# Kernel optimization log

Hardware: AMD Instinct MI355X
Metric: run time of the kernel (lower is better)

The kernel has to match this reference:

```python
import jax, jax.numpy as jnp
import numpy as np

NUM_NODES = 100000
EMB_DIM = 64
NUM_EDGES = 1280000
NUM_LAYERS = 3


def setup_inputs() -> dict:
    key = jax.random.key(0)
    k1, k2 = jax.random.split(key)
    edge_index = jax.random.randint(k1, (2, NUM_EDGES), 0, NUM_NODES, dtype=jnp.int32)
    emb = jax.random.normal(k2, (NUM_NODES, EMB_DIM), dtype=jnp.float32) * 0.01
    return {"edge_index": edge_index, "emb": emb}


def _lgconv_norm(edge_index):
    # PyG gcn_norm without self-loops: deg over destination nodes,
    # norm_e = deg[src]^-0.5 * deg[dst]^-0.5
    src, dst = edge_index[0], edge_index[1]
    deg = jax.ops.segment_sum(jnp.ones((edge_index.shape[1],), jnp.float32), dst,
                              num_segments=NUM_NODES)
    dinv = jnp.where(deg > 0, jax.lax.rsqrt(jnp.maximum(deg, 1.0)), 0.0)
    return src, dst, dinv[src] * dinv[dst]


def reference(edge_index, emb):
    src, dst, w = _lgconv_norm(edge_index)
    x = emb
    out = x
    for _ in range(NUM_LAYERS):
        # message: gather source embeddings, scale, scatter-add to destination
        x = jax.ops.segment_sum(x[src] * w[:, None], dst, num_segments=NUM_NODES)
        out = out + x
    return out / (NUM_LAYERS + 1)
```

## Files before the change

### kernel.cpp

```cpp
#include <hip/hip_runtime.h>

#define N_NODES 100000
#define EMB 64
#define N_EDGES 1280000
#define SCAN_TILE 1024

typedef unsigned long long u64;
typedef _Float16 f16;
typedef __attribute__((ext_vector_type(2))) _Float16 f16x2;

__global__ void deg_kernel(const int* __restrict__ dst, int* __restrict__ deg,
                           int* __restrict__ rank) {
    int t = blockIdx.x * blockDim.x + threadIdx.x;
    int e = t * 4;
    if (e + 3 < N_EDGES) {
        int4 d4 = *(const int4*)(dst + e);
        int4 r4;
        r4.x = atomicAdd(&deg[d4.x], 1);
        r4.y = atomicAdd(&deg[d4.y], 1);
        r4.z = atomicAdd(&deg[d4.z], 1);
        r4.w = atomicAdd(&deg[d4.w], 1);
        *(int4*)(rank + e) = r4;
    }
}

__global__ void norm_kernel(const int* __restrict__ deg, float* __restrict__ dinv,
                            float* __restrict__ rdinv) {
    int i = blockIdx.x * blockDim.x + threadIdx.x;
    if (i < N_NODES) {
        int d = deg[i];
        float fd = (float)d;
        dinv[i]  = (d > 0) ? rsqrtf(fd) : 0.0f;
        rdinv[i] = (d > 0) ? sqrtf(fd) : 0.0f;
    }
}

__global__ void y0_kernel(const float* __restrict__ emb, const float* __restrict__ dinv,
                          f16* __restrict__ y0) {
    int i = blockIdx.x * blockDim.x + threadIdx.x;
    const int n4 = N_NODES * EMB / 4;
    if (i < n4) {
        float dv = dinv[i >> 4];
        float4 v = ((const float4*)emb)[i];
        f16 h[4] = {(f16)(v.x * dv), (f16)(v.y * dv), (f16)(v.z * dv), (f16)(v.w * dv)};
        ((u64*)y0)[i] = *(const u64*)h;
    }
}

__global__ void scan1_kernel(const int* __restrict__ deg, int* __restrict__ local_scan,
                             int* __restrict__ block_sums) {
    __shared__ int lds[256];
    int base = blockIdx.x * SCAN_TILE;
    int vals[4];
    int tsum = 0;
#pragma unroll
    for (int k = 0; k < 4; ++k) {
        int i = base + threadIdx.x * 4 + k;
        vals[k] = (i < N_NODES) ? deg[i] : 0;
        tsum += vals[k];
    }
    lds[threadIdx.x] = tsum;
    __syncthreads();
    for (int off = 1; off < 256; off <<= 1) {
        int v = (threadIdx.x >= (unsigned)off) ? lds[threadIdx.x - off] : 0;
        __syncthreads();
        lds[threadIdx.x] += v;
        __syncthreads();
    }
    int texcl = lds[threadIdx.x] - tsum;
    if (threadIdx.x == 255) block_sums[blockIdx.x] = lds[255];
    int run = texcl;
#pragma unroll
    for (int k = 0; k < 4; ++k) {
        int i = base + threadIdx.x * 4 + k;
        if (i < N_NODES) local_scan[i] = run;
        run += vals[k];
    }
}

__global__ void scan2_kernel(int* __restrict__ block_sums, int nb) {
    __shared__ int lds[128];
    int v = (threadIdx.x < (unsigned)nb) ? block_sums[threadIdx.x] : 0;
    lds[threadIdx.x] = v;
    __syncthreads();
    for (int off = 1; off < 128; off <<= 1) {
        int t = (threadIdx.x >= (unsigned)off) ? lds[threadIdx.x - off] : 0;
        __syncthreads();
        lds[threadIdx.x] += t;
        __syncthreads();
    }
    if (threadIdx.x < (unsigned)nb) block_sums[threadIdx.x] = lds[threadIdx.x] - v;
}

__global__ void scan3_kernel(int* __restrict__ row_start, const int* __restrict__ block_sums) {
    int i = blockIdx.x * blockDim.x + threadIdx.x;
    if (i < N_NODES) {
        row_start[i] = row_start[i] + block_sums[i / SCAN_TILE];
    }
    if (i == 0) row_start[N_NODES] = N_EDGES;
}

__global__ void fill_kernel(const int* __restrict__ src, const int* __restrict__ dst,
                            const int* __restrict__ rank, const int* __restrict__ row_start,
                            int* __restrict__ col) {
    int t = blockIdx.x * blockDim.x + threadIdx.x;
    int e = t * 4;
    if (e + 3 < N_EDGES) {
        int4 d4 = *(const int4*)(dst + e);
        int4 r4 = *(const int4*)(rank + e);
        int4 s4 = *(const int4*)(src + e);
        col[row_start[d4.x] + r4.x] = s4.x;
        col[row_start[d4.y] + r4.y] = s4.y;
        col[row_start[d4.z] + r4.z] = s4.z;
        col[row_start[d4.w] + r4.w] = s4.w;
    }
}

template <bool FINAL>
__global__ void gather_kernel(const int* __restrict__ row_start, const int* __restrict__ col,
                              const float* __restrict__ dinv, const float* __restrict__ rdinv,
                              const f16* __restrict__ yin, f16* __restrict__ yout,
                              const float* __restrict__ emb,
                              const f16* __restrict__ y1, const f16* __restrict__ y2,
                              float* __restrict__ out) {
    unsigned int gid = blockIdx.x * blockDim.x + threadIdx.x;
    unsigned int row = gid >> 6;
    int lane = (int)(gid & 63u);
    int s = lane >> 5;
    int j = lane & 31;
    if (row >= N_NODES) return;
    int beg = row_start[row];
    int end = row_start[row + 1];
    const f16* yj = yin + 2 * j;
    float accx = 0.0f, accy = 0.0f;
    for (int cb = beg; cb < end; cb += 64) {
        int idx = cb + lane;
        int ci = 0;
        if (idx < end) ci = col[idx];
        int n = end - cb;
        if (n > 64) n = 64;
        int kk = 0;
        for (; kk + 8 <= n; kk += 8) {
            int c0 = __shfl(ci, kk + s);
            int c1 = __shfl(ci, kk + s + 2);
            int c2 = __shfl(ci, kk + s + 4);
            int c3 = __shfl(ci, kk + s + 6);
            unsigned u0 = *(const unsigned*)(yj + (unsigned)c0 * EMB);
            unsigned u1 = *(const unsigned*)(yj + (unsigned)c1 * EMB);
            unsigned u2 = *(const unsigned*)(yj + (unsigned)c2 * EMB);
            unsigned u3 = *(const unsigned*)(yj + (unsigned)c3 * EMB);
            f16x2 h0 = __builtin_bit_cast(f16x2, u0);
            f16x2 h1 = __builtin_bit_cast(f16x2, u1);
            f16x2 h2 = __builtin_bit_cast(f16x2, u2);
            f16x2 h3 = __builtin_bit_cast(f16x2, u3);
            accx += (float)h0.x + (float)h1.x + (float)h2.x + (float)h3.x;
            accy += (float)h0.y + (float)h1.y + (float)h2.y + (float)h3.y;
        }
        if (kk + 4 <= n) {
            int c0 = __shfl(ci, kk + s);
            int c1 = __shfl(ci, kk + s + 2);
            unsigned u0 = *(const unsigned*)(yj + (unsigned)c0 * EMB);
            unsigned u1 = *(const unsigned*)(yj + (unsigned)c1 * EMB);
            f16x2 h0 = __builtin_bit_cast(f16x2, u0);
            f16x2 h1 = __builtin_bit_cast(f16x2, u1);
            accx += (float)h0.x + (float)h1.x;
            accy += (float)h0.y + (float)h1.y;
            kk += 4;
        }
        for (; kk < n; ++kk) {
            int c = __shfl(ci, kk);
            if (s == (kk & 1)) {
                unsigned u = *(const unsigned*)(yj + (unsigned)c * EMB);
                f16x2 h = __builtin_bit_cast(f16x2, u);
                accx += (float)h.x;
                accy += (float)h.y;
            }
        }
    }
    accx += __shfl_xor(accx, 32);
    accy += __shfl_xor(accy, 32);
    if (s == 0) {
        float dv = dinv[row];
        unsigned int o = row * EMB + 2 * (unsigned)j;
        if (!FINAL) {
            float sc = dv * dv;
            f16x2 h;
            h.x = (f16)(accx * sc);
            h.y = (f16)(accy * sc);
            *(unsigned*)(yout + o) = __builtin_bit_cast(unsigned, h);
        } else {
            float rv = rdinv[row];
            float2 e2 = *(const float2*)(emb + o);
            f16x2 a = __builtin_bit_cast(f16x2, *(const unsigned*)(y1 + o));
            f16x2 b = __builtin_bit_cast(f16x2, *(const unsigned*)(y2 + o));
            float rx = 0.25f * (e2.x + rv * ((float)a.x + (float)b.x) + dv * accx);
            float ry = 0.25f * (e2.y + rv * ((float)a.y + (float)b.y) + dv * accy);
            __builtin_nontemporal_store(rx, out + o);
            __builtin_nontemporal_store(ry, out + o + 1);
        }
    }
}

extern "C" void kernel_launch(void* const* d_in, const int* in_sizes, int n_in,
                              void* d_out, int out_size, void* d_ws, size_t ws_size,
                              hipStream_t stream) {
    const int*   edge = (const int*)d_in[0];
    const int*   src  = edge;
    const int*   dst  = edge + N_EDGES;
    const float* emb  = (const float*)d_in[1];
    float*       out  = (float*)d_out;

    char* ws = (char*)d_ws;
    size_t off = 0;
    int* deg       = (int*)(ws + off); off += 400000;
    int* row_start = (int*)(ws + off); off += 400016;
    int* bsums     = (int*)(ws + off); off += 512;
    float* dinv    = (float*)(ws + off); off += 400000;
    float* rdinv   = (float*)(ws + off); off += 400000;
    int* col       = (int*)(ws + off); off += (size_t)N_EDGES * 4;
    f16* y0        = (f16*)(ws + off); off += (size_t)N_NODES * EMB * 2;
    f16* y1        = (f16*)(ws + off); off += (size_t)N_NODES * EMB * 2;
    f16* y2        = (f16*)(ws + off); off += (size_t)N_NODES * EMB * 2;

    int* rank      = (int*)y1;

    const int NB = (N_NODES + SCAN_TILE - 1) / SCAN_TILE;

    hipMemsetAsync(deg, 0, (size_t)N_NODES * sizeof(int), stream);
    deg_kernel<<<(N_EDGES / 4 + 255) / 256, 256, 0, stream>>>(dst, deg, rank);
    norm_kernel<<<(N_NODES + 255) / 256, 256, 0, stream>>>(deg, dinv, rdinv);
    y0_kernel<<<(N_NODES * EMB / 4 + 255) / 256, 256, 0, stream>>>(emb, dinv, y0);
    scan1_kernel<<<NB, 256, 0, stream>>>(deg, row_start, bsums);
    scan2_kernel<<<1, 128, 0, stream>>>(bsums, NB);
    scan3_kernel<<<(N_NODES + 255) / 256, 256, 0, stream>>>(row_start, bsums);
    fill_kernel<<<(N_EDGES / 4 + 255) / 256, 256, 0, stream>>>(src, dst, rank,
                                                               row_start, col);

    const unsigned int gthreads = (unsigned int)N_NODES * EMB;
    const int gblocks = (int)((gthreads + 255) / 256);
    gather_kernel<false><<<gblocks, 256, 0, stream>>>(row_start, col, dinv, rdinv,
                                                      y0, y1, emb, y1, y2, out);
    gather_kernel<false><<<gblocks, 256, 0, stream>>>(row_start, col, dinv, rdinv,
                                                      y1, y2, emb, y1, y2, out);
    gather_kernel<true><<<gblocks, 256, 0, stream>>>(row_start, col, dinv, rdinv,
                                                     y2, (f16*)0, emb, y1, y2, out);
}
```

Before: 308.4 us.

## Build CSR via two-level bucket sort with LDS-local degree counting

Replaces global-atomic degree counting and a random scatter fill with a bucketed counting sort. Edges are histogrammed into 512-node buckets, scanned, scattered into bucket order, then ranked per bucket with shared-memory atomics that also produce the degree. The CSR fill then reads bucket-ordered edges, so writes to col land in a narrow range. It adds four kernel launches, a single-block scan over roughly 61K entries, and an extra pass over the edge arrays in exchange for avoiding contended global atomics and scattered writes.

Result: slower. 366.2 us (+18.8%).

```diff
diff --git a/kernel.cpp b/kernel.cpp
--- a/kernel.cpp
+++ b/kernel.cpp
@@ -3,24 +3,115 @@
 #define N_NODES 100000
 #define EMB 64
 #define N_EDGES 1280000
+#define N_E4 (N_EDGES / 4)
 #define SCAN_TILE 1024
+
+#define NBUCK 196
+#define BUCK_SHIFT 9
+#define BUCK_NODES 512
+#define EPB 4096
+#define NBA 313
 
 typedef unsigned long long u64;
 typedef _Float16 f16;
 typedef __attribute__((ext_vector_type(2))) _Float16 f16x2;
 
-__global__ void deg_kernel(const int* __restrict__ dst, int* __restrict__ deg,
-                           int* __restrict__ rank) {
-    int t = blockIdx.x * blockDim.x + threadIdx.x;
-    int e = t * 4;
-    if (e + 3 < N_EDGES) {
-        int4 d4 = *(const int4*)(dst + e);
-        int4 r4;
-        r4.x = atomicAdd(&deg[d4.x], 1);
-        r4.y = atomicAdd(&deg[d4.y], 1);
-        r4.z = atomicAdd(&deg[d4.z], 1);
-        r4.w = atomicAdd(&deg[d4.w], 1);
-        *(int4*)(rank + e) = r4;
+__global__ void bucket_hist_kernel(const int* __restrict__ dst, int* __restrict__ hist) {
+    __shared__ int lh[NBUCK];
+    for (int i = threadIdx.x; i < NBUCK; i += 256) lh[i] = 0;
+    __syncthreads();
+#pragma unroll
+    for (int k = 0; k < 4; ++k) {
+        int q = blockIdx.x * 1024 + k * 256 + threadIdx.x;
+        if (q < N_E4) {
+            int4 d4 = ((const int4*)dst)[q];
+            atomicAdd(&lh[d4.x >> BUCK_SHIFT], 1);
+            atomicAdd(&lh[d4.y >> BUCK_SHIFT], 1);
+            atomicAdd(&lh[d4.z >> BUCK_SHIFT], 1);
+            atomicAdd(&lh[d4.w >> BUCK_SHIFT], 1);
+        }
+    }
+    __syncthreads();
+    for (int i = threadIdx.x; i < NBUCK; i += 256)
+        hist[i * NBA + blockIdx.x] = lh[i];
+}
+
+__global__ void bucket_scan_kernel(int* __restrict__ hist) {
+    const int TOT = NBUCK * NBA;
+    __shared__ int lds[1024];
+    int per = (TOT + 1023) / 1024;
+    int beg = threadIdx.x * per;
+    int end = beg + per; if (end > TOT) end = TOT;
+    int s = 0;
+    for (int i = beg; i < end && i < TOT; ++i) s += hist[i];
+    lds[threadIdx.x] = s;
+    __syncthreads();
+    for (int off = 1; off < 1024; off <<= 1) {
+        int v = (threadIdx.x >= (unsigned)off) ? lds[threadIdx.x - off] : 0;
+        __syncthreads();
+        lds[threadIdx.x] += v;
+        __syncthreads();
+    }
+    int run = lds[threadIdx.x] - s;
+    for (int i = beg; i < end && i < TOT; ++i) {
+        int v = hist[i];
+        hist[i] = run;
+        run += v;
+    }
+}
+
+__global__ void bucket_scatter_kernel(const int* __restrict__ src, const int* __restrict__ dst,
+                                      const int* __restrict__ hist,
+                                      int* __restrict__ bsrc, int* __restrict__ bdst) {
+    __shared__ int cur[NBUCK];
+    for (int i = threadIdx.x; i < NBUCK; i += 256)
+        cur[i] = hist[i * NBA + blockIdx.x];
+    __syncthreads();
+#pragma unroll
+    for (int k = 0; k < 4; ++k) {
+        int q = blockIdx.x * 1024 + k * 256 + threadIdx.x;
+        if (q < N_E4) {
+            int4 d4 = ((const int4*)dst)[q];
+            int4 s4 = ((const int4*)src)[q];
+            int p;
+            p = atomicAdd(&cur[d4.x >> BUCK_SHIFT], 1); bsrc[p] = s4.x; bdst[p] = d4.x;
+            p = atomicAdd(&cur[d4.y >> BUCK_SHIFT], 1); bsrc[p] = s4.y; bdst[p] = d4.y;
+            p = atomicAdd(&cur[d4.z >> BUCK_SHIFT], 1); bsrc[p] = s4.z; bdst[p] = d4.z;
+            p = atomicAdd(&cur[d4.w >> BUCK_SHIFT], 1); bsrc[p] = s4.w; bdst[p] = d4.w;
+        }
+    }
+}
+
+__global__ void bucket_rank_kernel(const int* __restrict__ hist, const int* __restrict__ bdst,
+                                   int* __restrict__ brank, int* __restrict__ deg) {
+    __shared__ int lh[BUCK_NODES];
+    int k = blockIdx.x;
+    int beg = hist[k * NBA];
+    int end = (k + 1 < NBUCK) ? hist[(k + 1) * NBA] : N_EDGES;
+    for (int i = threadIdx.x; i < BUCK_NODES; i += 256) lh[i] = 0;
+    __syncthreads();
+    for (int i = beg + threadIdx.x; i < end; i += 256) {
+        int d = bdst[i];
+        brank[i] = atomicAdd(&lh[d & (BUCK_NODES - 1)], 1);
+    }
+    __syncthreads();
+    int nbase = k * BUCK_NODES;
+    for (int i = threadIdx.x; i < BUCK_NODES; i += 256)
+        if (nbase + i < N_NODES) deg[nbase + i] = lh[i];
+}
+
+__global__ void csr_fill_kernel(const int* __restrict__ row_start, const int* __restrict__ bdst,
+                                const int* __restrict__ brank, const int* __restrict__ bsrc,
+                                int* __restrict__ col) {
+    int q = blockIdx.x * blockDim.x + threadIdx.x;
+    if (q < N_E4) {
+        int4 d4 = ((const int4*)bdst)[q];
+        int4 r4 = ((const int4*)brank)[q];
+        int4 s4 = ((const int4*)bsrc)[q];
+        col[row_start[d4.x] + r4.x] = s4.x;
+        col[row_start[d4.y] + r4.y] = s4.y;
+        col[row_start[d4.z] + r4.z] = s4.z;
+        col[row_start[d4.w] + r4.w] = s4.w;
     }
 }
 
@@ -98,22 +189,6 @@
         row_start[i] = row_start[i] + block_sums[i / SCAN_TILE];
     }
     if (i == 0) row_start[N_NODES] = N_EDGES;
-}
-
-__global__ void fill_kernel(const int* __restrict__ src, const int* __restrict__ dst,
-                            const int* __restrict__ rank, const int* __restrict__ row_start,
-                            int* __restrict__ col) {
-    int t = blockIdx.x * blockDim.x + threadIdx.x;
-    int e = t * 4;
-    if (e + 3 < N_EDGES) {
-        int4 d4 = *(const int4*)(dst + e);
-        int4 r4 = *(const int4*)(rank + e);
-        int4 s4 = *(const int4*)(src + e);
-        col[row_start[d4.x] + r4.x] = s4.x;
-        col[row_start[d4.y] + r4.y] = s4.y;
-        col[row_start[d4.z] + r4.z] = s4.z;
-        col[row_start[d4.w] + r4.w] = s4.w;
-    }
 }
 
 template <bool FINAL>
@@ -217,24 +292,29 @@
     int* bsums     = (int*)(ws + off); off += 512;
     float* dinv    = (float*)(ws + off); off += 400000;
     float* rdinv   = (float*)(ws + off); off += 400000;
+    int* hist      = (int*)(ws + off); off += (size_t)NBUCK * NBA * 4 + 16;
     int* col       = (int*)(ws + off); off += (size_t)N_EDGES * 4;
     f16* y0        = (f16*)(ws + off); off += (size_t)N_NODES * EMB * 2;
     f16* y1        = (f16*)(ws + off); off += (size_t)N_NODES * EMB * 2;
     f16* y2        = (f16*)(ws + off); off += (size_t)N_NODES * EMB * 2;
 
-    int* rank      = (int*)y1;
+    int* bsrc  = (int*)y1;
+    int* bdst  = (int*)((char*)y1 + (size_t)N_EDGES * 4);
+    int* brank = (int*)y2;
 
     const int NB = (N_NODES + SCAN_TILE - 1) / SCAN_TILE;
 
-    hipMemsetAsync(deg, 0, (size_t)N_NODES * sizeof(int), stream);
-    deg_kernel<<<(N_EDGES / 4 + 255) / 256, 256, 0, stream>>>(dst, deg, rank);
+    bucket_hist_kernel<<<NBA, 256, 0, stream>>>(dst, hist);
+    bucket_scan_kernel<<<1, 1024, 0, stream>>>(hist);
+    bucket_scatter_kernel<<<NBA, 256, 0, stream>>>(src, dst, hist, bsrc, bdst);
+    bucket_rank_kernel<<<NBUCK, 256, 0, stream>>>(hist, bdst, brank, deg);
     norm_kernel<<<(N_NODES + 255) / 256, 256, 0, stream>>>(deg, dinv, rdinv);
     y0_kernel<<<(N_NODES * EMB / 4 + 255) / 256, 256, 0, stream>>>(emb, dinv, y0);
     scan1_kernel<<<NB, 256, 0, stream>>>(deg, row_start, bsums);
     scan2_kernel<<<1, 128, 0, stream>>>(bsums, NB);
     scan3_kernel<<<(N_NODES + 255) / 256, 256, 0, stream>>>(row_start, bsums);
-    fill_kernel<<<(N_EDGES / 4 + 255) / 256, 256, 0, stream>>>(src, dst, rank,
-                                                               row_start, col);
+    csr_fill_kernel<<<(N_E4 + 255) / 256, 256, 0, stream>>>(row_start, bdst, brank,
+                                                            bsrc, col);
 
     const unsigned int gthreads = (unsigned int)N_NODES * EMB;
     const int gblocks = (int)((gthreads + 255) / 256);
```
